# Performance work log

Measured on AMD Instinct MI355X. Metric: run time of the kernel, lower is better.

The kernel has to match this reference:

```python
import jax, jax.numpy as jnp
import numpy as np

DIM = 768
N_HEADS = 12
HEAD_DIM = DIM // N_HEADS
BATCH = 2
SEQ = 4096


def setup_inputs() -> dict:
    key = jax.random.key(0)
    ks = jax.random.split(key, 9)
    s = 1.0 / np.sqrt(DIM)
    return {
        "x": jax.random.normal(ks[0], (BATCH, SEQ, DIM), dtype=jnp.float32),
        "Wq": jax.random.normal(ks[1], (DIM, DIM), dtype=jnp.float32) * s,
        "bq": jax.random.normal(ks[2], (DIM,), dtype=jnp.float32) * s,
        "Wk": jax.random.normal(ks[3], (DIM, DIM), dtype=jnp.float32) * s,
        "bk": jax.random.normal(ks[4], (DIM,), dtype=jnp.float32) * s,
        "Wv": jax.random.normal(ks[5], (DIM, DIM), dtype=jnp.float32) * s,
        "bv": jax.random.normal(ks[6], (DIM,), dtype=jnp.float32) * s,
        "Wo": jax.random.normal(ks[7], (DIM, DIM), dtype=jnp.float32) * s,
        "bo": jax.random.normal(ks[8], (DIM,), dtype=jnp.float32) * s,
    }


def reference(x, Wq, bq, Wk, bk, Wv, bv, Wo, bo):
    B, S, D = x.shape
    scale = 1.0 / np.sqrt(HEAD_DIM).astype(np.float32)
    # projections: [B,S,D] -> [B,H,S,Hd]
    def split_heads(t):
        return t.reshape(B, S, N_HEADS, HEAD_DIM).transpose(0, 2, 1, 3)
    q = split_heads(x @ Wq + bq)
    k = split_heads(x @ Wk + bk)
    v = split_heads(x @ Wv + bv)
    # full score matrix [B,H,S,S] as in the original (memory-bound)
    scores = jnp.einsum("bhqd,bhkd->bhqk", q, k) * scale
    attn = jax.nn.softmax(scores, axis=-1)
    out = jnp.einsum("bhqk,bhkd->bhqd", attn, v)
    out = out.transpose(0, 2, 1, 3).reshape(B, S, D)
    return out @ Wo + bo
```

## Files before the change

### kernel.cpp

```cpp
#include <hip/hip_runtime.h>
#include <hip/hip_bf16.h>
#include <math.h>

#define D_MODEL 768
#define NH 12
#define HD 64
#define BATCH 2
#define SEQ 4096
#define NROWS (BATCH * SEQ)

#define QSCALE 0.18033688011112042f

typedef __attribute__((ext_vector_type(8))) short short8;
typedef __attribute__((ext_vector_type(4))) short short4v;
typedef __attribute__((ext_vector_type(4))) float f32x4;
typedef __attribute__((ext_vector_type(16))) float f32x16;

__device__ inline unsigned short f2bf(float f) {
    __hip_bfloat16 h = __float2bfloat16(f);
    return *reinterpret_cast<unsigned short*>(&h);
}

__global__ __launch_bounds__(256) void convert_x_k(
    const float* __restrict__ x, unsigned short* __restrict__ xb)
{
    size_t i = ((size_t)blockIdx.x * 256 + threadIdx.x) * 8;
    float4 a = *(const float4*)(x + i);
    float4 b = *(const float4*)(x + i + 4);
    short8 o;
    o[0] = (short)f2bf(a.x); o[1] = (short)f2bf(a.y);
    o[2] = (short)f2bf(a.z); o[3] = (short)f2bf(a.w);
    o[4] = (short)f2bf(b.x); o[5] = (short)f2bf(b.y);
    o[6] = (short)f2bf(b.z); o[7] = (short)f2bf(b.w);
    *(short8*)(xb + i) = o;
}

__global__ __launch_bounds__(256) void convert_wt_k(
    const float* __restrict__ Wq, const float* __restrict__ Wk,
    const float* __restrict__ Wv, const float* __restrict__ Wo,
    unsigned short* __restrict__ wt)
{
    const float* W = (blockIdx.z == 0) ? Wq : (blockIdx.z == 1) ? Wk
                   : (blockIdx.z == 2) ? Wv : Wo;
    unsigned short* dst = wt + (size_t)blockIdx.z * D_MODEL * D_MODEL;
    __shared__ float tile[64][65];
    const int k0 = blockIdx.x * 64, n0 = blockIdx.y * 64;
    const int t = threadIdx.x;
    const int r = t >> 2, seg = t & 3;
    const float* src = W + (size_t)(k0 + r) * D_MODEL + n0 + seg * 16;
    #pragma unroll
    for (int i = 0; i < 4; ++i) {
        float4 v = *(const float4*)(src + i * 4);
        tile[r][seg * 16 + i * 4 + 0] = v.x;
        tile[r][seg * 16 + i * 4 + 1] = v.y;
        tile[r][seg * 16 + i * 4 + 2] = v.z;
        tile[r][seg * 16 + i * 4 + 3] = v.w;
    }
    __syncthreads();
    unsigned short* d = dst + (size_t)(n0 + r) * D_MODEL + k0 + seg * 16;
    short8 o0, o1;
    #pragma unroll
    for (int j = 0; j < 8; ++j) o0[j] = (short)f2bf(tile[seg * 16 + j][r]);
    #pragma unroll
    for (int j = 0; j < 8; ++j) o1[j] = (short)f2bf(tile[seg * 16 + 8 + j][r]);
    *(short8*)(d) = o0;
    *(short8*)(d + 8) = o1;
}

__global__ __launch_bounds__(256) void qkv_mfma_k(
    const unsigned short* __restrict__ xb,
    const unsigned short* __restrict__ wt,
    const float* __restrict__ bq, const float* __restrict__ bk,
    const float* __restrict__ bv,
    unsigned short* __restrict__ qb,
    unsigned short* __restrict__ kb,
    unsigned short* __restrict__ vtb)
{
    __shared__ unsigned short As[128][66];
    __shared__ unsigned short Bs[64][66];
    const int z = blockIdx.z;
    const unsigned short* Wt = wt + (size_t)z * D_MODEL * D_MODEL;
    const float* bias = (z == 0) ? bq : (z == 1) ? bk : bv;
    const int t = threadIdx.x;
    const int w = t >> 6, lane = t & 63, quad = lane >> 4, col = lane & 15;
    const int r0 = blockIdx.x * 128;
    const int c0 = blockIdx.y * 64;
    const int arow = t >> 1, ahalf = t & 1;
    const int brow = t >> 2, bseg = t & 3;

    f32x4 acc[2][4] = {};

    for (int kk = 0; kk < D_MODEL; kk += 64) {
        short8 areg[4], breg[2];
        const unsigned short* ag = xb + (size_t)(r0 + arow) * D_MODEL + kk + ahalf * 32;
        #pragma unroll
        for (int i = 0; i < 4; ++i) areg[i] = *(const short8*)(ag + i * 8);
        const unsigned short* bg = Wt + (size_t)(c0 + brow) * D_MODEL + kk + bseg * 16;
        breg[0] = *(const short8*)(bg);
        breg[1] = *(const short8*)(bg + 8);
        __syncthreads();
        #pragma unroll
        for (int i = 0; i < 4; ++i) *(short8*)&As[arow][ahalf * 32 + i * 8] = areg[i];
        *(short8*)&Bs[brow][bseg * 16] = breg[0];
        *(short8*)&Bs[brow][bseg * 16 + 8] = breg[1];
        __syncthreads();
        #pragma unroll
        for (int ks = 0; ks < 2; ++ks) {
            short8 af[2], bf[4];
            af[0] = *(const short8*)&As[w * 32 + col][ks * 32 + quad * 8];
            af[1] = *(const short8*)&As[w * 32 + 16 + col][ks * 32 + quad * 8];
            #pragma unroll
            for (int nt = 0; nt < 4; ++nt)
                bf[nt] = *(const short8*)&Bs[nt * 16 + col][ks * 32 + quad * 8];
            #pragma unroll
            for (int mt = 0; mt < 2; ++mt)
                #pragma unroll
                for (int nt = 0; nt < 4; ++nt)
                    acc[mt][nt] = __builtin_amdgcn_mfma_f32_16x16x32_bf16(
                        af[mt], bf[nt], acc[mt][nt], 0, 0, 0);
        }
    }

    const int h = blockIdx.y;
    #pragma unroll
    for (int nt = 0; nt < 4; ++nt) {
        const float bv_ = bias[c0 + nt * 16 + col];
        const int hd = nt * 16 + col;
        #pragma unroll
        for (int mt = 0; mt < 2; ++mt) {
            #pragma unroll
            for (int reg = 0; reg < 4; ++reg) {
                int r = r0 + w * 32 + mt * 16 + quad * 4 + reg;
                int b = r >> 12, s = r & (SEQ - 1);
                float val = acc[mt][nt][reg] + bv_;
                size_t bh = (size_t)(b * NH + h);
                if (z == 0)
                    qb[(bh * SEQ + s) * HD + hd] = f2bf(val * QSCALE);
                else if (z == 1)
                    kb[(bh * SEQ + s) * HD + hd] = f2bf(val);
                else
                    vtb[(bh * HD + hd) * SEQ + s] = f2bf(val);
            }
        }
    }
}

__global__ __launch_bounds__(256) void out_mfma_k(
    const unsigned short* __restrict__ ab,
    const unsigned short* __restrict__ wot,
    const float* __restrict__ bo,
    float* __restrict__ out)
{
    __shared__ unsigned short As[128][66];
    __shared__ unsigned short Bs[64][66];
    const int t = threadIdx.x;
    const int w = t >> 6, lane = t & 63, quad = lane >> 4, col = lane & 15;
    const int r0 = blockIdx.x * 128;
    const int c0 = blockIdx.y * 64;
    const int arow = t >> 1, ahalf = t & 1;
    const int brow = t >> 2, bseg = t & 3;

    f32x4 acc[2][4] = {};

    for (int kk = 0; kk < D_MODEL; kk += 64) {
        short8 areg[4], breg[2];
        const unsigned short* ag = ab + (size_t)(r0 + arow) * D_MODEL + kk + ahalf * 32;
        #pragma unroll
        for (int i = 0; i < 4; ++i) areg[i] = *(const short8*)(ag + i * 8);
        const unsigned short* bg = wot + (size_t)(c0 + brow) * D_MODEL + kk + bseg * 16;
        breg[0] = *(const short8*)(bg);
        breg[1] = *(const short8*)(bg + 8);
        __syncthreads();
        #pragma unroll
        for (int i = 0; i < 4; ++i) *(short8*)&As[arow][ahalf * 32 + i * 8] = areg[i];
        *(short8*)&Bs[brow][bseg * 16] = breg[0];
        *(short8*)&Bs[brow][bseg * 16 + 8] = breg[1];
        __syncthreads();
        #pragma unroll
        for (int ks = 0; ks < 2; ++ks) {
            short8 af[2], bf[4];
            af[0] = *(const short8*)&As[w * 32 + col][ks * 32 + quad * 8];
            af[1] = *(const short8*)&As[w * 32 + 16 + col][ks * 32 + quad * 8];
            #pragma unroll
            for (int nt = 0; nt < 4; ++nt)
                bf[nt] = *(const short8*)&Bs[nt * 16 + col][ks * 32 + quad * 8];
            #pragma unroll
            for (int mt = 0; mt < 2; ++mt)
                #pragma unroll
                for (int nt = 0; nt < 4; ++nt)
                    acc[mt][nt] = __builtin_amdgcn_mfma_f32_16x16x32_bf16(
                        af[mt], bf[nt], acc[mt][nt], 0, 0, 0);
        }
    }

    #pragma unroll
    for (int nt = 0; nt < 4; ++nt) {
        const float bv_ = bo[c0 + nt * 16 + col];
        #pragma unroll
        for (int mt = 0; mt < 2; ++mt) {
            #pragma unroll
            for (int reg = 0; reg < 4; ++reg) {
                int r = r0 + w * 32 + mt * 16 + quad * 4 + reg;
                out[(size_t)r * D_MODEL + c0 + nt * 16 + col] = acc[mt][nt][reg] + bv_;
            }
        }
    }
}

__global__ __launch_bounds__(256) void flash_mfma_k(
    const unsigned short* __restrict__ qb,
    const unsigned short* __restrict__ kb,
    const unsigned short* __restrict__ vtb,
    unsigned short* __restrict__ ab)
{
    __shared__ unsigned short Ks[64][66];
    __shared__ unsigned short Vts[64][66];
    __shared__ unsigned short Ps[4][32][66];

    const int t = threadIdx.x;
    const int w = t >> 6, lane = t & 63;
    const int l31 = lane & 31, hi = lane >> 5;
    const int q0 = blockIdx.x * 128;
    const int h = blockIdx.y, b = blockIdx.z;
    const size_t bh = (size_t)b * NH + h;
    const unsigned short* qg = qb + bh * SEQ * HD;
    const unsigned short* kg = kb + bh * SEQ * HD;
    const unsigned short* vg = vtb + bh * HD * SEQ;

    short8 qf[4];
    {
        const unsigned short* src = qg + (size_t)(q0 + w * 32 + l31) * HD + hi * 8;
        #pragma unroll
        for (int ks = 0; ks < 4; ++ks)
            qf[ks] = *(const short8*)(src + ks * 16);
    }

    f32x16 oacc[2] = {};
    float lsum = 0.f;
    const int srow = lane, sseg = w;

    for (int kt = 0; kt < SEQ; kt += 64) {
        const unsigned short* kp = kg + (size_t)(kt + srow) * HD + sseg * 16;
        short8 kr0 = *(const short8*)(kp);
        short8 kr1 = *(const short8*)(kp + 8);
        const unsigned short* vp = vg + (size_t)srow * SEQ + kt + sseg * 16;
        short8 vr0 = *(const short8*)(vp);
        short8 vr1 = *(const short8*)(vp + 8);
        __syncthreads();
        *(short8*)&Ks[srow][sseg * 16]      = kr0;
        *(short8*)&Ks[srow][sseg * 16 + 8]  = kr1;
        *(short8*)&Vts[srow][sseg * 16]     = vr0;
        *(short8*)&Vts[srow][sseg * 16 + 8] = vr1;
        __syncthreads();

        #pragma unroll
        for (int kti = 0; kti < 2; ++kti) {
            f32x16 s = {};
            #pragma unroll
            for (int ks = 0; ks < 4; ++ks) {
                short8 kf = *(const short8*)&Ks[kti * 32 + l31][ks * 16 + hi * 8];
                s = __builtin_amdgcn_mfma_f32_32x32x16_bf16(kf, qf[ks], s, 0, 0, 0);
            }
            #pragma unroll
            for (int rq = 0; rq < 4; ++rq) {
                float p0 = __builtin_amdgcn_exp2f(s[rq * 4 + 0]);
                float p1 = __builtin_amdgcn_exp2f(s[rq * 4 + 1]);
                float p2 = __builtin_amdgcn_exp2f(s[rq * 4 + 2]);
                float p3 = __builtin_amdgcn_exp2f(s[rq * 4 + 3]);
                lsum += (p0 + p1) + (p2 + p3);
                short4v pk;
                pk[0] = (short)f2bf(p0);
                pk[1] = (short)f2bf(p1);
                pk[2] = (short)f2bf(p2);
                pk[3] = (short)f2bf(p3);
                *(short4v*)&Ps[w][l31][kti * 32 + rq * 8 + hi * 4] = pk;
            }
        }

        #pragma unroll
        for (int ks = 0; ks < 4; ++ks) {
            short8 pf = *(const short8*)&Ps[w][l31][ks * 16 + hi * 8];
            #pragma unroll
            for (int dt = 0; dt < 2; ++dt) {
                short8 vf = *(const short8*)&Vts[dt * 32 + l31][ks * 16 + hi * 8];
                oacc[dt] = __builtin_amdgcn_mfma_f32_32x32x16_bf16(
                    vf, pf, oacc[dt], 0, 0, 0);
            }
        }
    }

    lsum += __shfl_xor(lsum, 32);
    float inv = 1.0f / lsum;
    int s = q0 + w * 32 + l31;
    unsigned short* dst = ab + ((size_t)b * SEQ + s) * D_MODEL + h * HD;
    #pragma unroll
    for (int dt = 0; dt < 2; ++dt) {
        #pragma unroll
        for (int rq = 0; rq < 4; ++rq) {
            short4v o4;
            o4[0] = (short)f2bf(oacc[dt][rq * 4 + 0] * inv);
            o4[1] = (short)f2bf(oacc[dt][rq * 4 + 1] * inv);
            o4[2] = (short)f2bf(oacc[dt][rq * 4 + 2] * inv);
            o4[3] = (short)f2bf(oacc[dt][rq * 4 + 3] * inv);
            *(short4v*)(dst + dt * 32 + rq * 8 + hi * 4) = o4;
        }
    }
}

extern "C" void kernel_launch(void* const* d_in, const int* in_sizes, int n_in,
                              void* d_out, int out_size, void* d_ws, size_t ws_size,
                              hipStream_t stream)
{
    const float* x  = (const float*)d_in[0];
    const float* Wq = (const float*)d_in[1];
    const float* bq = (const float*)d_in[2];
    const float* Wk = (const float*)d_in[3];
    const float* bk = (const float*)d_in[4];
    const float* Wv = (const float*)d_in[5];
    const float* bv = (const float*)d_in[6];
    const float* Wo = (const float*)d_in[7];
    const float* bo = (const float*)d_in[8];
    float* out = (float*)d_out;

    const size_t n_x  = (size_t)NROWS * D_MODEL;
    const size_t n_w  = (size_t)D_MODEL * D_MODEL;
    unsigned short* xb  = (unsigned short*)d_ws;
    unsigned short* wt  = xb + n_x;
    unsigned short* qb  = wt + 4 * n_w;
    unsigned short* kb  = qb + n_x;
    unsigned short* vtb = kb + n_x;
    unsigned short* ab  = vtb + n_x;
    const size_t need = ((size_t)4 * n_x + 4 * n_w + n_x) * sizeof(unsigned short);
    if (ws_size < need) return;

    convert_x_k<<<dim3((int)(n_x / 2048)), 256, 0, stream>>>(x, xb);
    convert_wt_k<<<dim3(12, 12, 4), 256, 0, stream>>>(Wq, Wk, Wv, Wo, wt);
    qkv_mfma_k<<<dim3(NROWS / 128, D_MODEL / 64, 3), 256, 0, stream>>>(
        xb, wt, bq, bk, bv, qb, kb, vtb);
    flash_mfma_k<<<dim3(SEQ / 128, NH, BATCH), 256, 0, stream>>>(qb, kb, vtb, ab);
    out_mfma_k<<<dim3(NROWS / 128, D_MODEL / 64), 256, 0, stream>>>(
        ab, wt + 3 * n_w, bo, out);
}
```

Baseline: 324.3 us.

## Double-buffer K/V tiles in flash attention to overlap global loads with MFMA

Makes the K and V^T shared-memory tiles double-buffered and issues the global loads for the next 64-key tile before computing on the current one. The loaded registers are written into the alternate buffer after the PV MFMAs, so each iteration needs one barrier instead of two. The aim is to hide global-memory latency behind compute. In exchange it doubles K/V LDS use and adds register pressure from holding the prefetched values, which may lower occupancy.

Result: slower. 334.1 us (+3.0%).

```diff
diff --git a/kernel.cpp b/kernel.cpp
--- a/kernel.cpp
+++ b/kernel.cpp
@@ -213,8 +213,8 @@
     const unsigned short* __restrict__ vtb,
     unsigned short* __restrict__ ab)
 {
-    __shared__ unsigned short Ks[64][66];
-    __shared__ unsigned short Vts[64][66];
+    __shared__ unsigned short Ks[2][64][66];
+    __shared__ unsigned short Vts[2][64][66];
     __shared__ unsigned short Ps[4][32][66];
 
     const int t = threadIdx.x;
@@ -239,26 +239,41 @@
     float lsum = 0.f;
     const int srow = lane, sseg = w;
 
-    for (int kt = 0; kt < SEQ; kt += 64) {
-        const unsigned short* kp = kg + (size_t)(kt + srow) * HD + sseg * 16;
+    {
+        const unsigned short* kp = kg + (size_t)srow * HD + sseg * 16;
         short8 kr0 = *(const short8*)(kp);
         short8 kr1 = *(const short8*)(kp + 8);
-        const unsigned short* vp = vg + (size_t)srow * SEQ + kt + sseg * 16;
+        const unsigned short* vp = vg + (size_t)srow * SEQ + sseg * 16;
         short8 vr0 = *(const short8*)(vp);
         short8 vr1 = *(const short8*)(vp + 8);
-        __syncthreads();
-        *(short8*)&Ks[srow][sseg * 16]      = kr0;
-        *(short8*)&Ks[srow][sseg * 16 + 8]  = kr1;
-        *(short8*)&Vts[srow][sseg * 16]     = vr0;
-        *(short8*)&Vts[srow][sseg * 16 + 8] = vr1;
-        __syncthreads();
+        *(short8*)&Ks[0][srow][sseg * 16]      = kr0;
+        *(short8*)&Ks[0][srow][sseg * 16 + 8]  = kr1;
+        *(short8*)&Vts[0][srow][sseg * 16]     = vr0;
+        *(short8*)&Vts[0][srow][sseg * 16 + 8] = vr1;
+        __syncthreads();
+    }
+
+    for (int kt = 0; kt < SEQ; kt += 64) {
+        const int cur = (kt >> 6) & 1;
+        const int nxt = cur ^ 1;
+        const bool more = (kt + 64) < SEQ;
+
+        short8 kr0, kr1, vr0, vr1;
+        if (more) {
+            const unsigned short* kp = kg + (size_t)(kt + 64 + srow) * HD + sseg * 16;
+            kr0 = *(const short8*)(kp);
+            kr1 = *(const short8*)(kp + 8);
+            const unsigned short* vp = vg + (size_t)srow * SEQ + (kt + 64) + sseg * 16;
+            vr0 = *(const short8*)(vp);
+            vr1 = *(const short8*)(vp + 8);
+        }
 
         #pragma unroll
         for (int kti = 0; kti < 2; ++kti) {
             f32x16 s = {};
             #pragma unroll
             for (int ks = 0; ks < 4; ++ks) {
-                short8 kf = *(const short8*)&Ks[kti * 32 + l31][ks * 16 + hi * 8];
+                short8 kf = *(const short8*)&Ks[cur][kti * 32 + l31][ks * 16 + hi * 8];
                 s = __builtin_amdgcn_mfma_f32_32x32x16_bf16(kf, qf[ks], s, 0, 0, 0);
             }
             #pragma unroll
@@ -282,10 +297,18 @@
             short8 pf = *(const short8*)&Ps[w][l31][ks * 16 + hi * 8];
             #pragma unroll
             for (int dt = 0; dt < 2; ++dt) {
-                short8 vf = *(const short8*)&Vts[dt * 32 + l31][ks * 16 + hi * 8];
+                short8 vf = *(const short8*)&Vts[cur][dt * 32 + l31][ks * 16 + hi * 8];
                 oacc[dt] = __builtin_amdgcn_mfma_f32_32x32x16_bf16(
                     vf, pf, oacc[dt], 0, 0, 0);
             }
+        }
+
+        if (more) {
+            *(short8*)&Ks[nxt][srow][sseg * 16]      = kr0;
+            *(short8*)&Ks[nxt][srow][sseg * 16 + 8]  = kr1;
+            *(short8*)&Vts[nxt][srow][sseg * 16]     = vr0;
+            *(short8*)&Vts[nxt][srow][sseg * 16 + 8] = vr1;
+            __syncthreads();
         }
     }
 
```
